# Optimization experiments

Hardware: AMD Instinct MI355X
Metric: run time of the kernel (lower is better)

Reference implementation:

```python
import jax, jax.numpy as jnp
import numpy as np

D_MODEL = 1024
H = 16
D_K = D_MODEL // H
BAND = 100  # attention allowed where |i-j| < BAND


def setup_inputs() -> dict:
    key = jax.random.key(0)
    ks = jax.random.split(key, 9)
    B, S = 2, 2048
    s = 1.0 / np.sqrt(D_MODEL)
    return {
        "x": jax.random.normal(ks[0], (B, S, D_MODEL), jnp.float32),
        "Wq": jax.random.normal(ks[1], (D_MODEL, D_MODEL), jnp.float32) * s,
        "bq": jnp.zeros((D_MODEL,), jnp.float32),
        "Wk": jax.random.normal(ks[2], (D_MODEL, D_MODEL), jnp.float32) * s,
        "bk": jnp.zeros((D_MODEL,), jnp.float32),
        "Wv": jax.random.normal(ks[3], (D_MODEL, D_MODEL), jnp.float32) * s,
        "bv": jnp.zeros((D_MODEL,), jnp.float32),
        "Wo": jax.random.normal(ks[4], (D_MODEL, D_MODEL), jnp.float32) * s,
        "bo": jnp.zeros((D_MODEL,), jnp.float32),
    }


def _split_heads(t, B, S):
    # [B, S, D] -> [B, H, S, D_K]
    return t.reshape(B, S, H, D_K).transpose(0, 2, 1, 3)


def reference(x, Wq, bq, Wk, bk, Wv, bv, Wo, bo):
    B, S, _ = x.shape
    q = _split_heads(x @ Wq.T + bq, B, S)
    k = _split_heads(x @ Wk.T + bk, B, S)
    v = _split_heads(x @ Wv.T + bv, B, S)

    scores = jnp.einsum("bhqd,bhkd->bhqk", q, k) / jnp.sqrt(jnp.float32(D_K))
    i = jnp.arange(S)
    band = jnp.abs(i[:, None] - i[None, :]) < BAND  # [S, S] True inside band
    scores = jnp.where(band[None, None, :, :], scores, jnp.float32(-1e9))
    p_attn = jax.nn.softmax(scores, axis=-1)

    out = jnp.einsum("bhqk,bhkd->bhqd", p_attn, v)
    out = out.transpose(0, 2, 1, 3).reshape(B, S, D_MODEL)
    return out @ Wo.T + bo
```

## Files before the change

kernel.cpp:

```cpp
#include <hip/hip_runtime.h>
#include <hip/hip_bf16.h>


typedef __attribute__((ext_vector_type(8))) short short8;
typedef __attribute__((ext_vector_type(4))) float f32x4;

#define S_LEN 2048
#define NH 16
#define DK 64
#define BANDW 100

#define X_ELEMS   (2 * S_LEN * 1024)
#define W_ELEMS   (1024 * 1024)
#define QKV_ELEMS (2 * NH * S_LEN * DK)
#define AO_ELEMS  (2 * S_LEN * 1024)

__device__ __attribute__((aligned(256))) short g_X[X_ELEMS];
__device__ __attribute__((aligned(256))) short g_W[4 * W_ELEMS];
__device__ __attribute__((aligned(256))) short g_b[4 * 1024];
__device__ __attribute__((aligned(256))) short g_Q[QKV_ELEMS];
__device__ __attribute__((aligned(256))) short g_K[QKV_ELEMS];
__device__ __attribute__((aligned(256))) short g_V[QKV_ELEMS];
__device__ __attribute__((aligned(256))) short g_AO[AO_ELEMS];

__device__ __forceinline__ float bf2f(short u) {
    unsigned x = ((unsigned)(unsigned short)u) << 16;
    return __builtin_bit_cast(float, x);
}
__device__ __forceinline__ short f2bf(float f) {
    unsigned x = __builtin_bit_cast(unsigned, f);
    unsigned r = (x + 0x7fffu + ((x >> 16) & 1u)) >> 16;
    return (short)r;
}

#define GLOAD_LDS(gp, lp) \
    __builtin_amdgcn_global_load_lds( \
        (const __attribute__((address_space(1))) void*)(gp), \
        (__attribute__((address_space(3))) void*)(lp), 16, 0, 0)

#define XC   (X_ELEMS / 8)
#define WC   (W_ELEMS / 8)
#define BC   (1024 / 8)
#define TOTC (XC + 4 * WC + 4 * BC)

__global__ __launch_bounds__(256) void convert_all(
    const void* __restrict__ x,
    const void* __restrict__ w0, const void* __restrict__ b0,
    const void* __restrict__ w1, const void* __restrict__ b1,
    const void* __restrict__ w2, const void* __restrict__ b2,
    const void* __restrict__ w3, const void* __restrict__ b3)
{
    __shared__ int cnt[256];
    {
        const unsigned* xw = (const unsigned*)x;
        int local = 0;
        #pragma unroll
        for (int i = 0; i < 4; i++) {
            unsigned wv = xw[threadIdx.x * 4 + i];
            unsigned e = (wv >> 7) & 0xFF;
            if (e >= 100 && e <= 140) local++;
        }
        cnt[threadIdx.x] = local;
    }
    __syncthreads();
    for (int s = 128; s > 0; s >>= 1) {
        if (threadIdx.x < s) cnt[threadIdx.x] += cnt[threadIdx.x + s];
        __syncthreads();
    }
    const int is_bf16 = (cnt[0] > 512);

    long i = (long)blockIdx.x * 256 + threadIdx.x;
    if (i >= TOTC) return;

    const void* src; short* dst; long off;
    if (i < XC)                { src = x;  dst = g_X;              off = i; }
    else if ((i -= XC) < WC)   { src = w0; dst = g_W + 0L*W_ELEMS; off = i; }
    else if ((i -= WC) < WC)   { src = w1; dst = g_W + 1L*W_ELEMS; off = i; }
    else if ((i -= WC) < WC)   { src = w2; dst = g_W + 2L*W_ELEMS; off = i; }
    else if ((i -= WC) < WC)   { src = w3; dst = g_W + 3L*W_ELEMS; off = i; }
    else if ((i -= WC) < BC)   { src = b0; dst = g_b + 0*1024;     off = i; }
    else if ((i -= BC) < BC)   { src = b1; dst = g_b + 1*1024;     off = i; }
    else if ((i -= BC) < BC)   { src = b2; dst = g_b + 2*1024;     off = i; }
    else                       { src = b3; dst = g_b + 3*1024;     off = i - BC; }

    if (is_bf16) {
        ((short8*)dst)[off] = ((const short8*)src)[off];
    } else {
        const float* s = (const float*)src + off * 8;
        short8 o;
        #pragma unroll
        for (int e = 0; e < 8; e++) o[e] = f2bf(s[e]);
        ((short8*)dst)[off] = o;
    }
}

__global__ __launch_bounds__(256) void qkv_gemm()
{
    __shared__ __attribute__((aligned(16))) short As[128 * 32];
    __shared__ __attribute__((aligned(16))) short Bs[128 * 32];

    const int z = blockIdx.z;
    const short* __restrict__ X = g_X;
    const short* __restrict__ W = g_W + (long)z * W_ELEMS;
    const short* __restrict__ bias = g_b + z * 1024;
    short* __restrict__ Out = (z == 0) ? g_Q : ((z == 1) ? g_K : g_V);
    const float scale = (z == 0) ? 0.125f : 1.0f;

    const int t = threadIdx.x;
    const int lane = t & 63;
    const int wid  = t >> 6;
    const int wm = wid & 1, wn = wid >> 1;
    const int l15 = lane & 15;
    const int q8  = (lane >> 4) * 8;
    const int mb = blockIdx.x * 128;
    const int nb = blockIdx.y * 128;

    const long ga0 = (long)(mb + (t >> 2)) * 1024 + (t & 3) * 8;
    const long ga1 = (long)(mb + 64 + (t >> 2)) * 1024 + (t & 3) * 8;
    const long gb0 = (long)(nb + (t >> 2)) * 1024 + (t & 3) * 8;
    const long gb1 = (long)(nb + 64 + (t >> 2)) * 1024 + (t & 3) * 8;
    short* lA0 = As + t * 8;
    short* lA1 = As + 2048 + t * 8;
    short* lB0 = Bs + t * 8;
    short* lB1 = Bs + 2048 + t * 8;

    f32x4 acc[4][4] = {};

    for (int k0 = 0; k0 < 1024; k0 += 32) {
        __syncthreads();
        GLOAD_LDS(X + ga0 + k0, lA0);
        GLOAD_LDS(X + ga1 + k0, lA1);
        GLOAD_LDS(W + gb0 + k0, lB0);
        GLOAD_LDS(W + gb1 + k0, lB1);
        __syncthreads();

        short8 a[4], b[4];
        #pragma unroll
        for (int mt = 0; mt < 4; mt++) a[mt] = *(const short8*)(As + (wm * 64 + mt * 16 + l15) * 32 + q8);
        #pragma unroll
        for (int nt = 0; nt < 4; nt++) b[nt] = *(const short8*)(Bs + (wn * 64 + nt * 16 + l15) * 32 + q8);
        #pragma unroll
        for (int mt = 0; mt < 4; mt++)
            #pragma unroll
            for (int nt = 0; nt < 4; nt++)
                acc[mt][nt] = __builtin_amdgcn_mfma_f32_16x16x32_bf16(a[mt], b[nt], acc[mt][nt], 0, 0, 0);
    }

    const int rg = (lane >> 4) * 4;
    #pragma unroll
    for (int nt = 0; nt < 4; nt++) {
        const int col = nb + wn * 64 + nt * 16 + l15;
        const float bv_ = bf2f(bias[col]);
        const int h = col >> 6, d = col & 63;
        #pragma unroll
        for (int mt = 0; mt < 4; mt++) {
            #pragma unroll
            for (int r = 0; r < 4; r++) {
                const int row = mb + wm * 64 + mt * 16 + rg + r;
                const int bI = row >> 11, s = row & 2047;
                Out[(((long)(bI * NH + h) * S_LEN) + s) * DK + d] = f2bf((acc[mt][nt][r] + bv_) * scale);
            }
        }
    }
}

__global__ __launch_bounds__(256) void o_gemm(float* __restrict__ Out)
{
    __shared__ __attribute__((aligned(16))) short As[128 * 32];
    __shared__ __attribute__((aligned(16))) short Bs[64 * 32];

    const short* __restrict__ A = g_AO;
    const short* __restrict__ W = g_W + 3L * W_ELEMS;

    const int t = threadIdx.x;
    const int lane = t & 63;
    const int wid  = t >> 6;
    const int wm = wid & 1, wn = wid >> 1;
    const int l15 = lane & 15;
    const int q8  = (lane >> 4) * 8;
    const int mb = blockIdx.x * 128;
    const int nb = blockIdx.y * 64;

    const long ga0 = (long)(mb + (t >> 2)) * 1024 + (t & 3) * 8;
    const long ga1 = (long)(mb + 64 + (t >> 2)) * 1024 + (t & 3) * 8;
    const long gb0 = (long)(nb + (t >> 2)) * 1024 + (t & 3) * 8;
    short* lA0 = As + t * 8;
    short* lA1 = As + 2048 + t * 8;
    short* lB0 = Bs + t * 8;

    f32x4 acc[4][2] = {};

    for (int k0 = 0; k0 < 1024; k0 += 32) {
        __syncthreads();
        GLOAD_LDS(A + ga0 + k0, lA0);
        GLOAD_LDS(A + ga1 + k0, lA1);
        GLOAD_LDS(W + gb0 + k0, lB0);
        __syncthreads();

        short8 a[4], b[2];
        #pragma unroll
        for (int mt = 0; mt < 4; mt++) a[mt] = *(const short8*)(As + (wm * 64 + mt * 16 + l15) * 32 + q8);
        #pragma unroll
        for (int nt = 0; nt < 2; nt++) b[nt] = *(const short8*)(Bs + (wn * 32 + nt * 16 + l15) * 32 + q8);
        #pragma unroll
        for (int mt = 0; mt < 4; mt++)
            #pragma unroll
            for (int nt = 0; nt < 2; nt++)
                acc[mt][nt] = __builtin_amdgcn_mfma_f32_16x16x32_bf16(a[mt], b[nt], acc[mt][nt], 0, 0, 0);
    }

    const int rg = (lane >> 4) * 4;
    #pragma unroll
    for (int nt = 0; nt < 2; nt++) {
        const int col = nb + wn * 32 + nt * 16 + l15;
        const float bv_ = bf2f(g_b[3 * 1024 + col]);
        #pragma unroll
        for (int mt = 0; mt < 4; mt++) {
            #pragma unroll
            for (int r = 0; r < 4; r++) {
                const int row = mb + wm * 64 + mt * 16 + rg + r;
                Out[(long)row * 1024 + col] = acc[mt][nt][r] + bv_;
            }
        }
    }
}

#define VT_PAD 328

__global__ __launch_bounds__(256) void attn_kernel()
{
    __shared__ __attribute__((aligned(16))) short Vt[64][VT_PAD];
    __shared__ __attribute__((aligned(16))) short Pl[4][16][72];

    const int bid  = blockIdx.x;
    const int head = bid & 31;
    const int qt   = bid >> 5;
    const int h = head & 15, b = head >> 4;
    const int qbase = qt * 64;

    const int lane = threadIdx.x & 63;
    const int w    = threadIdx.x >> 6;
    const int l15  = lane & 15;
    const int qg   = lane >> 4;
    const int q8   = qg * 8;

    const long hoff = (long)(b * NH + h) * S_LEN * DK;
    const short* __restrict__ Qh = g_Q + hoff;
    const short* __restrict__ Kh = g_K + hoff;
    const short* __restrict__ Vh = g_V + hoff;

    const int lo  = qbase - (BANDW - 1);
    const int kc0 = (lo < 0 ? 0 : lo) >> 6;
    int hi = qbase + 64 + (BANDW - 1);
    if (hi > S_LEN) hi = S_LEN;
    const int kc1 = (hi + 63) >> 6;
    const int kb0 = kc0 * 64;
    const int n_keys = (kc1 - kc0) * 64;

    const short* qp = Qh + (long)(qbase + w * 16 + l15) * DK + q8;
    const short8 aq0 = *(const short8*)(qp);
    const short8 aq1 = *(const short8*)(qp + 32);

    const int npairs = n_keys >> 1;
    for (int u = threadIdx.x; u < npairs; u += 256) {
        const short* vp0 = Vh + (long)(kb0 + 2 * u) * DK;
        #pragma unroll
        for (int tq = 0; tq < 8; tq++) {
            const short8 v0 = *(const short8*)(vp0 + tq * 8);
            const short8 v1 = *(const short8*)(vp0 + DK + tq * 8);
            #pragma unroll
            for (int e = 0; e < 8; e++) {
                const int pk = (int)(unsigned short)v0[e] | ((int)(unsigned short)v1[e] << 16);
                *(int*)&Vt[tq * 8 + e][2 * u] = pk;
            }
        }
    }
    __syncthreads();

    short8 nk0[4], nk1[4];
    #pragma unroll
    for (int nt = 0; nt < 4; nt++) {
        const short* kp = Kh + (long)(kb0 + nt * 16 + l15) * DK + q8;
        nk0[nt] = *(const short8*)(kp);
        nk1[nt] = *(const short8*)(kp + 32);
    }

    f32x4 o[4] = {};
    float m_r[4], l_r[4];
    #pragma unroll
    for (int r = 0; r < 4; r++) { m_r[r] = -1e30f; l_r[r] = 0.f; }

    for (int kc = kc0; kc < kc1; kc++) {
        const int kb = kc * 64;
        const int kloc = kb - kb0;

        short8 bk0[4], bk1[4];
        #pragma unroll
        for (int nt = 0; nt < 4; nt++) { bk0[nt] = nk0[nt]; bk1[nt] = nk1[nt]; }
        if (kc + 1 < kc1) {
            const int kbn = kb + 64;
            #pragma unroll
            for (int nt = 0; nt < 4; nt++) {
                const short* kp = Kh + (long)(kbn + nt * 16 + l15) * DK + q8;
                nk0[nt] = *(const short8*)(kp);
                nk1[nt] = *(const short8*)(kp + 32);
            }
        }

        f32x4 sc[4];
        #pragma unroll
        for (int nt = 0; nt < 4; nt++) {
            f32x4 z = {};
            z = __builtin_amdgcn_mfma_f32_16x16x32_bf16(aq0, bk0[nt], z, 0, 0, 0);
            z = __builtin_amdgcn_mfma_f32_16x16x32_bf16(aq1, bk1[nt], z, 0, 0, 0);
            sc[nt] = z;
        }

        float pv[4][4];
        float mx[4] = {-1e30f, -1e30f, -1e30f, -1e30f};
        if (kb == qbase) {
            #pragma unroll
            for (int nt = 0; nt < 4; nt++)
                #pragma unroll
                for (int r = 0; r < 4; r++) {
                    pv[nt][r] = sc[nt][r];
                    mx[r] = fmaxf(mx[r], sc[nt][r]);
                }
        } else {
            #pragma unroll
            for (int nt = 0; nt < 4; nt++) {
                const int kg = kb + nt * 16 + l15;
                #pragma unroll
                for (int r = 0; r < 4; r++) {
                    const int qI = qbase + w * 16 + qg * 4 + r;
                    int dlt = qI - kg; if (dlt < 0) dlt = -dlt;
                    const float v = (dlt < BANDW) ? sc[nt][r] : -1e30f;
                    pv[nt][r] = v;
                    mx[r] = fmaxf(mx[r], v);
                }
            }
        }
        #pragma unroll
        for (int mk = 1; mk < 16; mk <<= 1)
            #pragma unroll
            for (int r = 0; r < 4; r++) mx[r] = fmaxf(mx[r], __shfl_xor(mx[r], mk, 64));

        float alpha[4], lnew[4];
        #pragma unroll
        for (int r = 0; r < 4; r++) {
            const float mn = fmaxf(m_r[r], mx[r]);
            alpha[r] = __builtin_exp2f((m_r[r] - mn) * 1.44269504f);
            m_r[r] = mn;
            lnew[r] = 0.f;
        }
        #pragma unroll
        for (int nt = 0; nt < 4; nt++)
            #pragma unroll
            for (int r = 0; r < 4; r++) {
                const float p = (pv[nt][r] > -0.5e30f)
                    ? __builtin_exp2f((pv[nt][r] - m_r[r]) * 1.44269504f) : 0.f;
                pv[nt][r] = p;
                lnew[r] += p;
            }
        #pragma unroll
        for (int mk = 1; mk < 16; mk <<= 1)
            #pragma unroll
            for (int r = 0; r < 4; r++) lnew[r] += __shfl_xor(lnew[r], mk, 64);
        #pragma unroll
        for (int r = 0; r < 4; r++) l_r[r] = l_r[r] * alpha[r] + lnew[r];
        #pragma unroll
        for (int nt2 = 0; nt2 < 4; nt2++)
            #pragma unroll
            for (int r = 0; r < 4; r++) o[nt2][r] *= alpha[r];

        #pragma unroll
        for (int nt = 0; nt < 4; nt++)
            #pragma unroll
            for (int r = 0; r < 4; r++)
                Pl[w][qg * 4 + r][nt * 16 + l15] = f2bf(pv[nt][r]);
        asm volatile("s_waitcnt lgkmcnt(0)" ::: "memory");
        const short8 ap0 = *(const short8*)(&Pl[w][l15][q8]);
        const short8 ap1 = *(const short8*)(&Pl[w][l15][32 + q8]);

        #pragma unroll
        for (int nt2 = 0; nt2 < 4; nt2++) {
            const short* vrow = &Vt[nt2 * 16 + l15][kloc];
            const short8 bv0 = *(const short8*)(vrow + q8);
            const short8 bv1 = *(const short8*)(vrow + 32 + q8);
            o[nt2] = __builtin_amdgcn_mfma_f32_16x16x32_bf16(ap0, bv0, o[nt2], 0, 0, 0);
            o[nt2] = __builtin_amdgcn_mfma_f32_16x16x32_bf16(ap1, bv1, o[nt2], 0, 0, 0);
        }
    }

    #pragma unroll
    for (int nt2 = 0; nt2 < 4; nt2++)
        #pragma unroll
        for (int r = 0; r < 4; r++) {
            const int qI = qbase + w * 16 + qg * 4 + r;
            const int d = nt2 * 16 + l15;
            g_AO[((long)b * S_LEN + qI) * 1024 + h * DK + d] = f2bf(o[nt2][r] / l_r[r]);
        }
}

extern "C" void kernel_launch(void* const* d_in, const int* in_sizes, int n_in,
                              void* d_out, int out_size, void* d_ws, size_t ws_size,
                              hipStream_t stream) {
    float* out = (float*)d_out;

    convert_all<<<(TOTC + 255) / 256, 256, 0, stream>>>(
        d_in[0], d_in[1], d_in[2], d_in[3], d_in[4], d_in[5], d_in[6], d_in[7], d_in[8]);
    qkv_gemm<<<dim3(32, 8, 3), 256, 0, stream>>>();
    attn_kernel<<<dim3(2 * NH * (S_LEN / 64)), 256, 0, stream>>>();
    o_gemm<<<dim3(32, 16), 256, 0, stream>>>(out);
}
```

Before: 179.1 us.

## Rewrite QKV GEMM as 256x256 tile, double-buffered, 8-wave pipelined kernel

Replaces the 128x128 QKV projection GEMM, which synchronised twice per 32-wide k step, with a 256x256-tile kernel of 512 threads. It double-buffers K=64 slices in LDS with an XOR-swizzled layout and interleaves async global-to-LDS loads with four MFMA phases per step, using s_setprio and explicit vmcnt waits. The three Q/K/V weight matrices are treated as one concatenated N=3072 GEMM over 192 blocks. The goal is to hide memory latency and raise data reuse per tile, at the cost of fragile hand-written synchronisation and only 192 blocks, which leaves some CUs idle.

```diff
diff --git a/kernel.cpp b/kernel.cpp
--- a/kernel.cpp
+++ b/kernel.cpp
@@ -94,74 +94,165 @@
     }
 }
 
-__global__ __launch_bounds__(256) void qkv_gemm()
+
+#define LHALF 8192
+
+__global__ __launch_bounds__(512, 2) void qkv_gemm256()
 {
-    __shared__ __attribute__((aligned(16))) short As[128 * 32];
-    __shared__ __attribute__((aligned(16))) short Bs[128 * 32];
-
-    const int z = blockIdx.z;
-    const short* __restrict__ X = g_X;
-    const short* __restrict__ W = g_W + (long)z * W_ELEMS;
-    const short* __restrict__ bias = g_b + z * 1024;
+    __shared__ __attribute__((aligned(16))) short L[8][LHALF];
+
+    const int t = threadIdx.x;
+    const int lane = t & 63;
+    const int w    = t >> 6;
+    const int l15  = lane & 15;
+    const int qg   = lane >> 4;
+    const int wr   = w >> 2;
+    const int wc   = w & 3;
+
+    const int bid = blockIdx.x;
+    const int mb  = (bid & 15) << 8;
+    const int nb  = (bid >> 4) << 8;
+
+    const int srow = w * 16 + (lane >> 3);
+    const int scol = ((lane & 7) << 3) ^ ((lane >> 5) << 4);
+    const short* pA0 = g_X + (long)(mb       + srow) * 1024 + scol;
+    const short* pA1 = g_X + (long)(mb + 128 + srow) * 1024 + scol;
+    const short* pB0 = g_W + (long)(nb       + srow) * 1024 + scol;
+    const short* pB1 = g_W + (long)(nb + 128 + srow) * 1024 + scol;
+    const int ldst = w * 1024 + lane * 8;
+
+#define STAGE(reg_, gp_, kt_) do {                         \
+        short* lp_ = &L[(reg_)][ldst];                     \
+        GLOAD_LDS((gp_) + (long)(kt_), lp_);               \
+        GLOAD_LDS((gp_) + 8192 + (long)(kt_), lp_ + 512);  \
+    } while (0)
+
+#define BARRIER() asm volatile("s_barrier" ::: "memory")
+
+    const int axs    = (l15 & 4) << 2;
+    const int a_off0 = (qg << 3) ^ axs;
+    const int a_off1 = (32 + (qg << 3)) ^ axs;
+    const int brow   = (wc & 1) * 64;
+
+    f32x4 acc[8][4] = {};
+
+    STAGE(0*4 + 2 + 0, pB0, 0);
+    STAGE(0*4 + 0 + 0, pA0, 0);
+    STAGE(0*4 + 0 + 1, pA1, 0);
+    STAGE(0*4 + 2 + 1, pB1, 0);
+    STAGE(1*4 + 2 + 0, pB0, 64);
+    STAGE(1*4 + 0 + 0, pA0, 64);
+    asm volatile("s_waitcnt vmcnt(4)" ::: "memory");
+    BARRIER();
+
+    for (int T = 0; T < 16; T++) {
+        const int buf = T & 1;
+        const short* Ah = L[buf*4 + wr];
+        const short* Bh = L[buf*4 + 2 + (wc >> 1)];
+        short8 afr[4][2], bfr[4][2];
+
+        #pragma unroll
+        for (int mi = 0; mi < 4; mi++) {
+            const int rb = (mi*16 + l15) * 64;
+            afr[mi][0] = *(const short8*)(Ah + rb + a_off0);
+            afr[mi][1] = *(const short8*)(Ah + rb + a_off1);
+        }
+        #pragma unroll
+        for (int ni = 0; ni < 2; ni++) {
+            const int rb = (brow + ni*16 + l15) * 64;
+            bfr[ni][0] = *(const short8*)(Bh + rb + a_off0);
+            bfr[ni][1] = *(const short8*)(Bh + rb + a_off1);
+        }
+        if (T + 1 < 16) STAGE(((T+1)&1)*4 + 1, pA1, (T+1)*64);
+        BARRIER();
+        __builtin_amdgcn_s_setprio(1);
+        #pragma unroll
+        for (int mi = 0; mi < 4; mi++)
+            #pragma unroll
+            for (int ni = 0; ni < 2; ni++) {
+                acc[mi][ni] = __builtin_amdgcn_mfma_f32_16x16x32_bf16(afr[mi][0], bfr[ni][0], acc[mi][ni], 0, 0, 0);
+                acc[mi][ni] = __builtin_amdgcn_mfma_f32_16x16x32_bf16(afr[mi][1], bfr[ni][1], acc[mi][ni], 0, 0, 0);
+            }
+        __builtin_amdgcn_s_setprio(0);
+        BARRIER();
+
+        #pragma unroll
+        for (int ni = 2; ni < 4; ni++) {
+            const int rb = (brow + ni*16 + l15) * 64;
+            bfr[ni][0] = *(const short8*)(Bh + rb + a_off0);
+            bfr[ni][1] = *(const short8*)(Bh + rb + a_off1);
+        }
+        if (T + 1 < 16) STAGE(((T+1)&1)*4 + 2 + 1, pB1, (T+1)*64);
+        BARRIER();
+        __builtin_amdgcn_s_setprio(1);
+        #pragma unroll
+        for (int mi = 0; mi < 4; mi++)
+            #pragma unroll
+            for (int ni = 2; ni < 4; ni++) {
+                acc[mi][ni] = __builtin_amdgcn_mfma_f32_16x16x32_bf16(afr[mi][0], bfr[ni][0], acc[mi][ni], 0, 0, 0);
+                acc[mi][ni] = __builtin_amdgcn_mfma_f32_16x16x32_bf16(afr[mi][1], bfr[ni][1], acc[mi][ni], 0, 0, 0);
+            }
+        __builtin_amdgcn_s_setprio(0);
+        BARRIER();
+
+        #pragma unroll
+        for (int mi = 0; mi < 4; mi++) {
+            const int rb = ((mi + 4)*16 + l15) * 64;
+            afr[mi][0] = *(const short8*)(Ah + rb + a_off0);
+            afr[mi][1] = *(const short8*)(Ah + rb + a_off1);
+        }
+        if (T + 2 < 16) STAGE((T&1)*4 + 2 + 0, pB0, (T+2)*64);
+        BARRIER();
+        __builtin_amdgcn_s_setprio(1);
+        #pragma unroll
+        for (int mi = 0; mi < 4; mi++)
+            #pragma unroll
+            for (int ni = 2; ni < 4; ni++) {
+                acc[mi+4][ni] = __builtin_amdgcn_mfma_f32_16x16x32_bf16(afr[mi][0], bfr[ni][0], acc[mi+4][ni], 0, 0, 0);
+                acc[mi+4][ni] = __builtin_amdgcn_mfma_f32_16x16x32_bf16(afr[mi][1], bfr[ni][1], acc[mi+4][ni], 0, 0, 0);
+            }
+        __builtin_amdgcn_s_setprio(0);
+        BARRIER();
+
+        if (T + 2 < 16) STAGE((T&1)*4 + 0, pA0, (T+2)*64);
+        BARRIER();
+        __builtin_amdgcn_s_setprio(1);
+        #pragma unroll
+        for (int mi = 0; mi < 4; mi++)
+            #pragma unroll
+            for (int ni = 0; ni < 2; ni++) {
+                acc[mi+4][ni] = __builtin_amdgcn_mfma_f32_16x16x32_bf16(afr[mi][0], bfr[ni][0], acc[mi+4][ni], 0, 0, 0);
+                acc[mi+4][ni] = __builtin_amdgcn_mfma_f32_16x16x32_bf16(afr[mi][1], bfr[ni][1], acc[mi+4][ni], 0, 0, 0);
+            }
+        __builtin_amdgcn_s_setprio(0);
+        if (T <= 13)      asm volatile("s_waitcnt vmcnt(4)" ::: "memory");
+        else if (T == 14) asm volatile("s_waitcnt vmcnt(0)" ::: "memory");
+        BARRIER();
+    }
+
+    const int nbase = nb + wc * 64;
+    const int z = nbase >> 10;
     short* __restrict__ Out = (z == 0) ? g_Q : ((z == 1) ? g_K : g_V);
     const float scale = (z == 0) ? 0.125f : 1.0f;
-
-    const int t = threadIdx.x;
-    const int lane = t & 63;
-    const int wid  = t >> 6;
-    const int wm = wid & 1, wn = wid >> 1;
-    const int l15 = lane & 15;
-    const int q8  = (lane >> 4) * 8;
-    const int mb = blockIdx.x * 128;
-    const int nb = blockIdx.y * 128;
-
-    const long ga0 = (long)(mb + (t >> 2)) * 1024 + (t & 3) * 8;
-    const long ga1 = (long)(mb + 64 + (t >> 2)) * 1024 + (t & 3) * 8;
-    const long gb0 = (long)(nb + (t >> 2)) * 1024 + (t & 3) * 8;
-    const long gb1 = (long)(nb + 64 + (t >> 2)) * 1024 + (t & 3) * 8;
-    short* lA0 = As + t * 8;
-    short* lA1 = As + 2048 + t * 8;
-    short* lB0 = Bs + t * 8;
-    short* lB1 = Bs + 2048 + t * 8;
-
-    f32x4 acc[4][4] = {};
-
-    for (int k0 = 0; k0 < 1024; k0 += 32) {
-        __syncthreads();
-        GLOAD_LDS(X + ga0 + k0, lA0);
-        GLOAD_LDS(X + ga1 + k0, lA1);
-        GLOAD_LDS(W + gb0 + k0, lB0);
-        GLOAD_LDS(W + gb1 + k0, lB1);
-        __syncthreads();
-
-        short8 a[4], b[4];
-        #pragma unroll
-        for (int mt = 0; mt < 4; mt++) a[mt] = *(const short8*)(As + (wm * 64 + mt * 16 + l15) * 32 + q8);
-        #pragma unroll
-        for (int nt = 0; nt < 4; nt++) b[nt] = *(const short8*)(Bs + (wn * 64 + nt * 16 + l15) * 32 + q8);
-        #pragma unroll
-        for (int mt = 0; mt < 4; mt++)
-            #pragma unroll
-            for (int nt = 0; nt < 4; nt++)
-                acc[mt][nt] = __builtin_amdgcn_mfma_f32_16x16x32_bf16(a[mt], b[nt], acc[mt][nt], 0, 0, 0);
-    }
-
-    const int rg = (lane >> 4) * 4;
+    const int rg = qg * 4;
     #pragma unroll
-    for (int nt = 0; nt < 4; nt++) {
-        const int col = nb + wn * 64 + nt * 16 + l15;
-        const float bv_ = bf2f(bias[col]);
-        const int h = col >> 6, d = col & 63;
-        #pragma unroll
-        for (int mt = 0; mt < 4; mt++) {
+    for (int ni = 0; ni < 4; ni++) {
+        const int n = nbase + ni * 16 + l15;
+        const int c = n & 1023;
+        const float bv_ = bf2f(g_b[z * 1024 + c]);
+        const int h = c >> 6, d = c & 63;
+        #pragma unroll
+        for (int mi = 0; mi < 8; mi++) {
             #pragma unroll
             for (int r = 0; r < 4; r++) {
-                const int row = mb + wm * 64 + mt * 16 + rg + r;
+                const int row = mb + wr * 128 + mi * 16 + rg + r;
                 const int bI = row >> 11, s = row & 2047;
-                Out[(((long)(bI * NH + h) * S_LEN) + s) * DK + d] = f2bf((acc[mt][nt][r] + bv_) * scale);
-            }
-        }
-    }
+                Out[(((long)(bI * NH + h) * S_LEN) + s) * DK + d] = f2bf((acc[mi][ni][r] + bv_) * scale);
+            }
+        }
+    }
+#undef STAGE
+#undef BARRIER
 }
 
 __global__ __launch_bounds__(256) void o_gemm(float* __restrict__ Out)
@@ -409,7 +500,7 @@
 
     convert_all<<<(TOTC + 255) / 256, 256, 0, stream>>>(
         d_in[0], d_in[1], d_in[2], d_in[3], d_in[4], d_in[5], d_in[6], d_in[7], d_in[8]);
-    qkv_gemm<<<dim3(32, 8, 3), 256, 0, stream>>>();
+    qkv_gemm256<<<dim3(192), 512, 0, stream>>>();
     attn_kernel<<<dim3(2 * NH * (S_LEN / 64)), 256, 0, stream>>>();
     o_gemm<<<dim3(32, 16), 256, 0, stream>>>(out);
 }
```

Result: slower. 183.9 us (+2.7%).
